# Kernel optimization log

Hardware: AMD Instinct MI355X
Metric: run time of the kernel (lower is better)

The kernel has to match this reference:

```python
import jax, jax.numpy as jnp
import numpy as np

M, N, IN_DIM, NITER = 32, 32, 1024, 100
ALPHA, SIGMA = 0.3, 16.0  # sigma default = max(m, n) / 2
BATCH = 16384


def setup_inputs() -> dict:
    key = jax.random.key(0)
    k1, k2 = jax.random.split(key)
    x = jax.random.normal(k1, (BATCH, IN_DIM), dtype=jnp.float32)
    weights = jax.random.normal(k2, (IN_DIM, M * N), dtype=jnp.float32)
    ii, jj = jnp.meshgrid(jnp.arange(M), jnp.arange(N), indexing='ij')
    locations = jnp.stack([ii.ravel(), jj.ravel()], axis=1).astype(jnp.int32)  # (m*n, 2), row-major like the generator
    return {"x": x, "weights": weights, "locations": locations, "current_iter": 10}


def reference(x, weights, locations, current_iter):
    # x: (B, in_dim); weights: (in_dim, m*n); locations: (m*n, 2)
    B = x.shape[0]
    # Euclidean distances from each sample to each neuron, via ||a-b||^2 expansion
    x2 = jnp.sum(x * x, axis=1, keepdims=True)            # (B, 1)
    w2 = jnp.sum(weights * weights, axis=0)[None, :]      # (1, m*n)
    d2 = jnp.clip(x2 + w2 - 2.0 * (x @ weights), 0.0, None)
    dists = jnp.sqrt(d2)                                  # (B, m*n)
    loss_per = jnp.min(dists, axis=1)                     # (B,)
    bmu_index = jnp.argmin(dists, axis=1)                 # (B,)
    iter_correction = 1.0 - current_iter / NITER
    lr = ALPHA * iter_correction
    sigma = SIGMA * iter_correction
    loc_f = locations.astype(jnp.float32)                 # (m*n, 2)
    bmu_loc = loc_f[bmu_index]                            # (B, 2)
    # squared grid distance of every neuron to each sample's BMU
    dsq = jnp.sum((loc_f[None, :, :] - bmu_loc[:, None, :]) ** 2, axis=2)  # (B, m*n)
    lr_locations = jnp.exp(-dsq / (sigma * sigma)) * lr   # (B, m*n)
    # delta[i,k] = (1/B) * sum_b lr_locations[b,k] * (x[b,i] - weights[i,k])
    # computed without materializing the (B, in_dim, m*n) broadcast tensor
    pos = jnp.einsum('bk,bi->ik', lr_locations, x)        # (in_dim, m*n)
    neg = weights * jnp.sum(lr_locations, axis=0)[None, :]
    delta = (pos - neg) / B
    new_weights = weights + delta
    loss = jnp.sum(loss_per) / B
    return loss, new_weights
```

## Files before the change

### kernel.cpp

```cpp
#include <hip/hip_runtime.h>

typedef unsigned short u16;
typedef short bf16x8 __attribute__((ext_vector_type(8)));
typedef float f32x4 __attribute__((ext_vector_type(4)));

#define BATCH   16384
#define INDIM   1024
#define KNEUR   1024

__device__ __forceinline__ u16 f2bf(float f) {
  union { float f; unsigned u; } v; v.f = f;
  unsigned r = v.u + 0x7FFFu + ((v.u >> 16) & 1u);
  return (u16)(r >> 16);
}
__device__ __forceinline__ float bf2f(u16 h) {
  union { unsigned u; float f; } v; v.u = ((unsigned)h) << 16; return v.f;
}

#define GLDS(gp, lp) __builtin_amdgcn_global_load_lds( \
  (const __attribute__((address_space(1))) void*)(gp), \
  (__attribute__((address_space(3))) void*)(lp), 16, 0, 0)

#define RAWBAR() __builtin_amdgcn_s_barrier()
#define LGKM0() do { asm volatile("s_waitcnt lgkmcnt(0)" ::: "memory"); \
                     __builtin_amdgcn_sched_barrier(0); } while (0)
#define LGKM8() asm volatile("s_waitcnt lgkmcnt(8)" ::: "memory")
#define VMC6() asm volatile("s_waitcnt vmcnt(6)" ::: "memory")
#define VMC0() asm volatile("s_waitcnt vmcnt(0)" ::: "memory")

__global__ __launch_bounds__(256)
void k_prep(const float* __restrict__ x, u16* __restrict__ xb, float* __restrict__ x2,
            const float* __restrict__ w, u16* __restrict__ wt, float* __restrict__ w2,
            const int* __restrict__ loc, const int* __restrict__ itp,
            u16* __restrict__ Tb, float* __restrict__ Tf,
            float* __restrict__ Xf, int* __restrict__ cntcur, float* __restrict__ S) {
  __shared__ float tile[64][65];
  __shared__ float red[4][64];
  int bid = blockIdx.x;
  int t = threadIdx.x;
  if (bid < 4096) {
    int row = bid * 4 + (t >> 6);
    int l = t & 63;
    const float* xr = x + (size_t)row * INDIM;
    u16* xbr = xb + (size_t)row * INDIM;
    float s = 0.f;
    #pragma unroll
    for (int seg = 0; seg < 4; ++seg) {
      float4 v = *(const float4*)(xr + seg * 256 + l * 4);
      ushort4 o; o.x = f2bf(v.x); o.y = f2bf(v.y); o.z = f2bf(v.z); o.w = f2bf(v.w);
      *(ushort4*)(xbr + seg * 256 + l * 4) = o;
      s += v.x * v.x + v.y * v.y + v.z * v.z + v.w * v.w;
    }
    for (int m = 32; m; m >>= 1) s += __shfl_xor(s, m, 64);
    if (l == 0) x2[row] = s;
  } else if (bid < 8192) {
    int id = (bid - 4096) * 256 + t;
    int c = id >> 10, k = id & 1023;
    float corr = 1.f - (float)itp[0] / 100.f;
    float lr = 0.3f * corr;
    float sig = 16.f * corr;
    float inv_s2 = 1.f / (sig * sig);
    int di = loc[2 * c] - loc[2 * k];
    int dj = loc[2 * c + 1] - loc[2 * k + 1];
    float v = lr * __expf(-(float)(di * di + dj * dj) * inv_s2);
    Tf[id] = v;
    Tb[id] = f2bf(v);
    Xf[id] = 0.f;
    if (id < 2304) cntcur[id] = 0;
    if (id < 1024) S[id] = 0.f;
  } else if (bid < 8448) {
    int bb = bid - 8192;
    int bi = bb & 15;
    int bj = bb >> 4;
    int tx = t & 63, ty = t >> 6;
    int i0 = bj * 64, k0 = bi * 64;
    for (int r = ty; r < 64; r += 4)
      tile[r][tx] = w[(size_t)(i0 + r) * KNEUR + k0 + tx];
    __syncthreads();
    for (int r = ty; r < 64; r += 4)
      wt[(size_t)(k0 + r) * INDIM + i0 + tx] = f2bf(tile[tx][r]);
  } else {
    int tx = t & 63, ty = t >> 6;
    int k = (bid - 8448) * 64 + tx;
    float s = 0.f;
    for (int i = ty * 256; i < ty * 256 + 256; ++i) {
      float v = w[(size_t)i * KNEUR + k];
      s += v * v;
    }
    red[ty][tx] = s;
    __syncthreads();
    if (ty == 0) w2[k] = red[0][tx] + red[1][tx] + red[2][tx] + red[3][tx];
  }
}

__global__ __launch_bounds__(512, 2)
void k_gemm1_8p(const u16* __restrict__ A, const u16* __restrict__ Bm,
                const float* __restrict__ x2, const float* __restrict__ w2,
                float* __restrict__ pmin, int* __restrict__ pidx) {
  __shared__ __align__(16) u16 lds[2][2][2][128 * 64];
  __shared__ float s_rv[2][256];
  __shared__ int   s_ri[2][256];

  int bid = blockIdx.x;
  int swz = (bid & 7) * 32 + (bid >> 3);
  int mb = swz >> 2, nb = swz & 3;
  int tid = threadIdx.x;
  int lane = tid & 63;
  int wm = (tid >> 6) >> 1, wn = (tid >> 6) & 1;

  const size_t rowA0 = (size_t)mb * 256;
  const size_t rowB0 = (size_t)nb * 256;

  auto STAGE = [&](int u, int op, int qh) {
    if (u >= 16) return;
    const u16* src = (op == 0) ? (A + (rowA0 + qh * 128) * 1024)
                               : (Bm + (rowB0 + qh * 128) * 1024);
    int k0 = u * 64;
    u16* dst0 = &lds[u & 1][op][qh][0];
    #pragma unroll
    for (int j = 0; j < 2; ++j) {
      int s = j * 512 + tid;
      int r = s >> 3;
      int cs = (s & 7) ^ (r & 7);
      GLDS(src + (size_t)r * 1024 + k0 + cs * 8, dst0 + (size_t)s * 8);
    }
  };
  auto LDA = [&](bf16x8 (&a)[2][2], int db, int qm) {
    #pragma unroll
    for (int mt = 0; mt < 2; ++mt)
      #pragma unroll
      for (int kk = 0; kk < 2; ++kk) {
        int row = wm * 32 + mt * 16 + (lane & 15);
        int ch = (kk * 4 + (lane >> 4)) ^ (row & 7);
        a[mt][kk] = *(const bf16x8*)(&lds[db][0][qm][row * 64 + ch * 8]);
      }
  };
  auto LDB = [&](bf16x8 (&b)[4][2], int db, int qn) {
    #pragma unroll
    for (int nt = 0; nt < 4; ++nt)
      #pragma unroll
      for (int kk = 0; kk < 2; ++kk) {
        int row = wn * 64 + nt * 16 + (lane & 15);
        int ch = (kk * 4 + (lane >> 4)) ^ (row & 7);
        b[nt][kk] = *(const bf16x8*)(&lds[db][1][qn][row * 64 + ch * 8]);
      }
  };

  f32x4 acc[2][2][2][4];
  #pragma unroll
  for (int i = 0; i < 2; ++i)
    #pragma unroll
    for (int j = 0; j < 2; ++j)
      #pragma unroll
      for (int m = 0; m < 2; ++m)
        #pragma unroll
        for (int n = 0; n < 4; ++n) {
          acc[i][j][m][n][0] = 0.f; acc[i][j][m][n][1] = 0.f;
          acc[i][j][m][n][2] = 0.f; acc[i][j][m][n][3] = 0.f;
        }

  bf16x8 a[2][2], b0[4][2], b1[4][2];

  #define PHASE(accq, av, bv) do { \
    __builtin_amdgcn_s_setprio(1); \
    _Pragma("unroll") \
    for (int mt = 0; mt < 2; ++mt) \
      _Pragma("unroll") \
      for (int nt = 0; nt < 4; ++nt) \
        _Pragma("unroll") \
        for (int kk = 0; kk < 2; ++kk) \
          accq[mt][nt] = __builtin_amdgcn_mfma_f32_16x16x32_bf16(av[mt][kk], bv[nt][kk], accq[mt][nt], 0, 0, 0); \
    __builtin_amdgcn_s_setprio(0); \
  } while (0)

  STAGE(0, 0, 0); STAGE(0, 1, 1); STAGE(0, 0, 1); STAGE(0, 1, 0);
  STAGE(1, 0, 0); STAGE(1, 1, 1); STAGE(1, 0, 1);
  VMC6();
  RAWBAR();

  for (int t = 0; t < 16; ++t) {
    int db = t & 1;
    LDA(a, db, 0); LDB(b0, db, 0);
    STAGE(t + 1, 1, 0);
    LGKM8();
    RAWBAR(); LGKM0();
    PHASE(acc[0][0], a, b0);
    RAWBAR();
    LDB(b1, db, 1);
    STAGE(t + 2, 0, 0);
    RAWBAR(); LGKM0();
    PHASE(acc[0][1], a, b1);
    RAWBAR();
    LDA(a, db, 1);
    STAGE(t + 2, 1, 1);
    RAWBAR(); LGKM0();
    PHASE(acc[1][1], a, b1);
    RAWBAR();
    STAGE(t + 2, 0, 1);
    RAWBAR(); LGKM0();
    PHASE(acc[1][0], a, b0);
    if (t < 14) { VMC6(); } else { VMC0(); }
    RAWBAR();
  }

  int g = lane >> 4, li = lane & 15;
  #pragma unroll
  for (int qm = 0; qm < 2; ++qm)
    #pragma unroll
    for (int mt = 0; mt < 2; ++mt)
      #pragma unroll
      for (int rr = 0; rr < 4; ++rr) {
        int lrow = qm * 128 + wm * 32 + mt * 16 + g * 4 + rr;
        float xv = x2[rowA0 + lrow];
        float v = 1e30f; int vi = 0x7fffffff;
        #pragma unroll
        for (int qn = 0; qn < 2; ++qn)
          #pragma unroll
          for (int nt = 0; nt < 4; ++nt) {
            int col = (int)rowB0 + qn * 128 + wn * 64 + nt * 16 + li;
            float d2 = xv + w2[col] - 2.f * acc[qm][qn][mt][nt][rr];
            if (d2 < v) { v = d2; vi = col; }
          }
        #pragma unroll
        for (int m = 1; m < 16; m <<= 1) {
          float ov = __shfl_xor(v, m, 64);
          int oi = __shfl_xor(vi, m, 64);
          if (ov < v || (ov == v && oi < vi)) { v = ov; vi = oi; }
        }
        if (li == 0) { s_rv[wn][lrow] = v; s_ri[wn][lrow] = vi; }
      }
  __syncthreads();
  if (tid < 256) {
    float v0 = s_rv[0][tid], v1 = s_rv[1][tid];
    int i0 = s_ri[0][tid], i1 = s_ri[1][tid];
    float v = v0; int vi = i0;
    if (v1 < v0 || (v1 == v0 && i1 < i0)) { v = v1; vi = i1; }
    size_t brow = rowA0 + tid;
    pmin[brow * 4 + nb] = v;
    pidx[brow * 4 + nb] = vi;
  }
  #undef PHASE
}

__global__ __launch_bounds__(256, 2)
void k_gemm2f(const u16* __restrict__ A, const u16* __restrict__ Bm,
              const float* __restrict__ w, const float* __restrict__ S,
              float* __restrict__ outw) {
  __shared__ __align__(16) u16 ldsA[2][64 * 64];
  __shared__ __align__(16) u16 ldsB[2][64 * 64];

  int bid = blockIdx.x;
  int mb = bid >> 4, nb = bid & 15;
  int tid = threadIdx.x;
  int lane = tid & 63;
  int wid = tid >> 6;
  int wr = wid >> 1, wc = wid & 1;

  const size_t rowA0 = (size_t)mb * 64;
  const size_t rowB0 = (size_t)nb * 64;

  auto STAGE2 = [&](int u, int buf) {
    int k0 = u * 64;
    #pragma unroll
    for (int j = 0; j < 2; ++j) {
      int s = j * 256 + tid;
      int r = s >> 3;
      int cs = (s & 7) ^ (r & 7);
      GLDS(A + (rowA0 + r) * 1024 + k0 + cs * 8, &ldsA[buf][s * 8]);
      GLDS(Bm + (rowB0 + r) * 1024 + k0 + cs * 8, &ldsB[buf][s * 8]);
    }
  };

  f32x4 acc[2][2];
  #pragma unroll
  for (int i = 0; i < 2; ++i)
    #pragma unroll
    for (int j = 0; j < 2; ++j) { acc[i][j][0] = 0.f; acc[i][j][1] = 0.f; acc[i][j][2] = 0.f; acc[i][j][3] = 0.f; }

  STAGE2(0, 0);
  VMC0();
  RAWBAR();

  for (int t = 0; t < 16; ++t) {
    int buf = t & 1;
    if (t < 15) STAGE2(t + 1, buf ^ 1);
    bf16x8 af[2][2], bfr[2][2];
    #pragma unroll
    for (int mt = 0; mt < 2; ++mt)
      #pragma unroll
      for (int kk = 0; kk < 2; ++kk) {
        int row = wr * 32 + mt * 16 + (lane & 15);
        int ch = (kk * 4 + (lane >> 4)) ^ (row & 7);
        af[mt][kk] = *(const bf16x8*)(&ldsA[buf][row * 64 + ch * 8]);
      }
    #pragma unroll
    for (int nt = 0; nt < 2; ++nt)
      #pragma unroll
      for (int kk = 0; kk < 2; ++kk) {
        int row = wc * 32 + nt * 16 + (lane & 15);
        int ch = (kk * 4 + (lane >> 4)) ^ (row & 7);
        bfr[nt][kk] = *(const bf16x8*)(&ldsB[buf][row * 64 + ch * 8]);
      }
    LGKM0();
    __builtin_amdgcn_s_setprio(1);
    #pragma unroll
    for (int mt = 0; mt < 2; ++mt)
      #pragma unroll
      for (int nt = 0; nt < 2; ++nt)
        #pragma unroll
        for (int kk = 0; kk < 2; ++kk)
          acc[mt][nt] = __builtin_amdgcn_mfma_f32_16x16x32_bf16(af[mt][kk], bfr[nt][kk], acc[mt][nt], 0, 0, 0);
    __builtin_amdgcn_s_setprio(0);
    if (t < 15) { VMC0(); RAWBAR(); }
  }

  const float invB = 1.f / (float)BATCH;
  #pragma unroll
  for (int mt = 0; mt < 2; ++mt)
    #pragma unroll
    for (int nt = 0; nt < 2; ++nt)
      #pragma unroll
      for (int r = 0; r < 4; ++r) {
        int i = (int)rowA0 + wr * 32 + mt * 16 + (lane >> 4) * 4 + r;
        int k = (int)rowB0 + wc * 32 + nt * 16 + (lane & 15);
        float wv = w[(size_t)i * KNEUR + k];
        outw[(size_t)i * KNEUR + k] = wv + (acc[mt][nt][r] - wv * S[k]) * invB;
      }
}

__global__ void k_bmu_scan(const float* __restrict__ pmin, const int* __restrict__ pidx,
                           int* __restrict__ bmu, float* __restrict__ lpart,
                           int* __restrict__ cnt, int* __restrict__ ticket,
                           int* __restrict__ cursor, float* __restrict__ cntf,
                           float* __restrict__ out) {
  int t = threadIdx.x;
  int b = blockIdx.x * 256 + t;
  float v = 1e30f; int vi = 0;
  #pragma unroll
  for (int j = 0; j < 4; ++j) {
    float pv = pmin[(size_t)b * 4 + j];
    if (pv < v) { v = pv; vi = pidx[(size_t)b * 4 + j]; }
  }
  bmu[b] = vi;
  atomicAdd(&cnt[vi], 1);
  float d = sqrtf(fmaxf(v, 0.f));
  __shared__ float red[256];
  red[t] = d;
  __syncthreads();
  for (int s = 128; s > 0; s >>= 1) {
    if (t < s) red[t] += red[t + s];
    __syncthreads();
  }
  if (t == 0) lpart[blockIdx.x] = red[0];

  __threadfence();
  __shared__ int is_last;
  if (t == 0) is_last = (atomicAdd(ticket, 1) == 63);
  __syncthreads();
  if (!is_last) return;

  __shared__ int sc[256];
  int4 c4 = *(const int4*)(cnt + 4 * t);
  int tsum = c4.x + c4.y + c4.z + c4.w;
  sc[t] = tsum;
  __syncthreads();
  for (int off = 1; off < 256; off <<= 1) {
    int val = sc[t];
    int add = (t >= off) ? sc[t - off] : 0;
    __syncthreads();
    sc[t] = val + add;
    __syncthreads();
  }
  int excl = sc[t] - tsum;
  cursor[4 * t + 0] = excl;
  cursor[4 * t + 1] = excl + c4.x;
  cursor[4 * t + 2] = excl + c4.x + c4.y;
  cursor[4 * t + 3] = excl + c4.x + c4.y + c4.z;
  cntf[4 * t + 0] = (float)c4.x;
  cntf[4 * t + 1] = (float)c4.y;
  cntf[4 * t + 2] = (float)c4.z;
  cntf[4 * t + 3] = (float)c4.w;
  if (t < 64) {
    float l = lpart[t];
    for (int m = 32; m; m >>= 1) l += __shfl_xor(l, m, 64);
    if (t == 0) out[0] = l * (1.f / (float)BATCH);
  }
}

__global__ void k_place_S(const int* __restrict__ bmu, int* __restrict__ cursor,
                          int* __restrict__ perm,
                          const float* __restrict__ cntf, const float* __restrict__ Tf,
                          float* __restrict__ S) {
  int bid = blockIdx.x;
  int t = threadIdx.x;
  if (bid < 64) {
    int b = bid * 256 + t;
    int c = bmu[b];
    int p = atomicAdd(&cursor[c], 1);
    perm[p] = b;
  } else {
    int chunk = bid - 64;
    int cchunk = chunk >> 2;
    int kb = chunk & 3;
    int k = kb * 256 + t;
    float s = 0.f;
    for (int c = cchunk * 64; c < cchunk * 64 + 64; ++c)
      s += cntf[c] * Tf[(size_t)c * KNEUR + k];
    atomicAdd(&S[k], s);
  }
}

__global__ __launch_bounds__(256)
void k_xsum2(const int* __restrict__ perm, const int* __restrict__ bmu,
             const u16* __restrict__ xb, float* __restrict__ Xf) {
  int t = threadIdx.x;
  int m0 = blockIdx.x * 32;
  int pm[32], cl[32];
  #pragma unroll
  for (int j = 0; j < 32; ++j) pm[j] = perm[m0 + j];
  #pragma unroll
  for (int j = 0; j < 32; ++j) cl[j] = bmu[pm[j]];
  float a0 = 0.f, a1 = 0.f, a2 = 0.f, a3 = 0.f;
  int ccur = cl[0];
  #pragma unroll
  for (int j = 0; j < 32; ++j) {
    if (cl[j] != ccur) {
      float* p = Xf + (size_t)ccur * INDIM + 4 * t;
      atomicAdd(p + 0, a0); atomicAdd(p + 1, a1);
      atomicAdd(p + 2, a2); atomicAdd(p + 3, a3);
      a0 = a1 = a2 = a3 = 0.f;
      ccur = cl[j];
    }
    ushort4 v = *(const ushort4*)(xb + (size_t)pm[j] * INDIM + t * 4);
    a0 += bf2f(v.x); a1 += bf2f(v.y); a2 += bf2f(v.z); a3 += bf2f(v.w);
  }
  float* p = Xf + (size_t)ccur * INDIM + 4 * t;
  atomicAdd(p + 0, a0); atomicAdd(p + 1, a1);
  atomicAdd(p + 2, a2); atomicAdd(p + 3, a3);
}

__global__ void k_trans(const float* __restrict__ Xf, u16* __restrict__ xst) {
  int bid = blockIdx.x;
  int t = threadIdx.x;
  __shared__ float tile[64][65];
  int bc = bid & 15;
  int bi = bid >> 4;
  int tx = t & 63, ty = t >> 6;
  int c0 = bc * 64, i0 = bi * 64;
  for (int r = ty; r < 64; r += 4)
    tile[r][tx] = Xf[(size_t)(c0 + r) * INDIM + i0 + tx];
  __syncthreads();
  for (int r = ty; r < 64; r += 4)
    xst[(size_t)(i0 + r) * KNEUR + c0 + tx] = f2bf(tile[tx][r]);
}

extern "C" void kernel_launch(void* const* d_in, const int* in_sizes, int n_in,
                              void* d_out, int out_size, void* d_ws, size_t ws_size,
                              hipStream_t stream) {
  const float* x = (const float*)d_in[0];
  const float* w = (const float*)d_in[1];
  const int* loc = (const int*)d_in[2];
  const int* it = (const int*)d_in[3];
  float* out = (float*)d_out;

  char* ws = (char*)d_ws;
  size_t off = 0;
  auto alloc = [&](size_t bytes) -> void* {
    void* p = ws + off;
    off += (bytes + 255) & ~(size_t)255;
    return p;
  };
  u16* xb    = (u16*)  alloc((size_t)BATCH * INDIM * 2);
  u16* wt    = (u16*)  alloc((size_t)KNEUR * INDIM * 2);
  u16* Tb    = (u16*)  alloc((size_t)KNEUR * KNEUR * 2);
  float* Tf  = (float*)alloc((size_t)KNEUR * KNEUR * 4);
  u16* xst   = (u16*)  alloc((size_t)INDIM * KNEUR * 2);
  float* x2  = (float*)alloc((size_t)BATCH * 4);
  float* w2  = (float*)alloc((size_t)KNEUR * 4);
  float* pmin= (float*)alloc((size_t)BATCH * 4 * 4);
  int* pidx  = (int*)  alloc((size_t)BATCH * 4 * 4);
  int* bmu   = (int*)  alloc((size_t)BATCH * 4);
  float* cntf= (float*)alloc((size_t)KNEUR * 4);
  float* S   = (float*)alloc((size_t)KNEUR * 4);
  float* lpart=(float*)alloc(64 * 4);
  float* Xf  = (float*)alloc((size_t)KNEUR * INDIM * 4);
  int* cntcur= (int*)  alloc((size_t)2304 * 4);
  int* perm  = (int*)  alloc((size_t)BATCH * 4);
  if (off > ws_size) return;

  int* cnt = cntcur;
  int* cursor = cntcur + KNEUR;
  int* ticket = cntcur + 2 * KNEUR;
  float* outw = out + 1;

  k_prep<<<8464, 256, 0, stream>>>(x, xb, x2, w, wt, w2, loc, it, Tb, Tf, Xf, cntcur, S);
  k_gemm1_8p<<<256, 512, 0, stream>>>(xb, wt, x2, w2, pmin, pidx);
  k_bmu_scan<<<64, 256, 0, stream>>>(pmin, pidx, bmu, lpart, cnt, ticket, cursor, cntf, out);
  k_place_S<<<128, 256, 0, stream>>>(bmu, cursor, perm, cntf, Tf, S);
  k_xsum2<<<BATCH / 32, 256, 0, stream>>>(perm, bmu, xb, Xf);
  k_trans<<<256, 256, 0, stream>>>(Xf, xst);
  k_gemm2f<<<256, 256, 0, stream>>>(xst, Tb, w, S, outw);
}
```

Measured before the change: 135.1 us.

## Quantize x and weights to FP8 e4m3 for the distance GEMM and x sums

The prep kernel now encodes x and the transposed weights as FP8 e4m3 with a software encoder, replacing bf16. The distance GEMM loads 16-byte FP8 chunks into half-size LDS tiles with an adjusted swizzle and uses 16x16x32 fp8 MFMAs. Launch bounds now ask for 4 blocks per CU, and wait counts are retuned for one global-to-LDS load per stage. The x column-sum kernel reads the FP8 copy, so traffic halves and MFMA throughput rises. In exchange, the much coarser precision can flip BMU argmin choices and add error to the weight update.

```diff
diff --git a/kernel.cpp b/kernel.cpp
--- a/kernel.cpp
+++ b/kernel.cpp
@@ -1,6 +1,7 @@
 #include <hip/hip_runtime.h>
 
 typedef unsigned short u16;
+typedef unsigned char u8;
 typedef short bf16x8 __attribute__((ext_vector_type(8)));
 typedef float f32x4 __attribute__((ext_vector_type(4)));
 
@@ -17,6 +18,32 @@
   union { unsigned u; float f; } v; v.u = ((unsigned)h) << 16; return v.f;
 }
 
+__device__ __forceinline__ u8 f2fp8(float f) {
+  float af = fabsf(f);
+  unsigned sign = (__float_as_uint(f) >> 24) & 0x80u;
+  if (af >= 448.f) return (u8)(sign | 0x7E);
+  if (af < 0.015625f) {
+    int q = (int)rintf(af * 512.f);
+    return (u8)(sign | (unsigned)q);
+  }
+  unsigned b = __float_as_uint(af);
+  int e = (int)((b >> 23) & 0xFF) - 127;
+  unsigned m = b & 0x7FFFFFu;
+  unsigned keep = m >> 20;
+  unsigned rest = m & 0xFFFFFu;
+  keep += (rest > 0x80000u) || (rest == 0x80000u && (keep & 1u));
+  unsigned ef = (unsigned)(e + 7);
+  if (keep == 8u) { keep = 0u; ef++; }
+  if (ef >= 16u) return (u8)(sign | 0x7E);
+  return (u8)(sign | (ef << 3) | keep);
+}
+__device__ __forceinline__ float fp8dec(u8 v) {
+  int e = (v >> 3) & 15, m = v & 7;
+  float mag = e ? (float)(8 + m) * __uint_as_float((unsigned)(e + 117) << 23)
+                : (float)m * 0x1p-9f;
+  return (v & 0x80) ? -mag : mag;
+}
+
 #define GLDS(gp, lp) __builtin_amdgcn_global_load_lds( \
   (const __attribute__((address_space(1))) void*)(gp), \
   (__attribute__((address_space(3))) void*)(lp), 16, 0, 0)
@@ -24,13 +51,12 @@
 #define RAWBAR() __builtin_amdgcn_s_barrier()
 #define LGKM0() do { asm volatile("s_waitcnt lgkmcnt(0)" ::: "memory"); \
                      __builtin_amdgcn_sched_barrier(0); } while (0)
-#define LGKM8() asm volatile("s_waitcnt lgkmcnt(8)" ::: "memory")
-#define VMC6() asm volatile("s_waitcnt vmcnt(6)" ::: "memory")
+#define VMC3() asm volatile("s_waitcnt vmcnt(3)" ::: "memory")
 #define VMC0() asm volatile("s_waitcnt vmcnt(0)" ::: "memory")
 
 __global__ __launch_bounds__(256)
-void k_prep(const float* __restrict__ x, u16* __restrict__ xb, float* __restrict__ x2,
-            const float* __restrict__ w, u16* __restrict__ wt, float* __restrict__ w2,
+void k_prep(const float* __restrict__ x, u8* __restrict__ xb, float* __restrict__ x2,
+            const float* __restrict__ w, u8* __restrict__ wt, float* __restrict__ w2,
             const int* __restrict__ loc, const int* __restrict__ itp,
             u16* __restrict__ Tb, float* __restrict__ Tf,
             float* __restrict__ Xf, int* __restrict__ cntcur, float* __restrict__ S) {
@@ -42,13 +68,13 @@
     int row = bid * 4 + (t >> 6);
     int l = t & 63;
     const float* xr = x + (size_t)row * INDIM;
-    u16* xbr = xb + (size_t)row * INDIM;
+    u8* xbr = xb + (size_t)row * INDIM;
     float s = 0.f;
     #pragma unroll
     for (int seg = 0; seg < 4; ++seg) {
       float4 v = *(const float4*)(xr + seg * 256 + l * 4);
-      ushort4 o; o.x = f2bf(v.x); o.y = f2bf(v.y); o.z = f2bf(v.z); o.w = f2bf(v.w);
-      *(ushort4*)(xbr + seg * 256 + l * 4) = o;
+      uchar4 o; o.x = f2fp8(v.x); o.y = f2fp8(v.y); o.z = f2fp8(v.z); o.w = f2fp8(v.w);
+      *(uchar4*)(xbr + seg * 256 + l * 4) = o;
       s += v.x * v.x + v.y * v.y + v.z * v.z + v.w * v.w;
     }
     for (int m = 32; m; m >>= 1) s += __shfl_xor(s, m, 64);
@@ -78,7 +104,7 @@
       tile[r][tx] = w[(size_t)(i0 + r) * KNEUR + k0 + tx];
     __syncthreads();
     for (int r = ty; r < 64; r += 4)
-      wt[(size_t)(k0 + r) * INDIM + i0 + tx] = f2bf(tile[tx][r]);
+      wt[(size_t)(k0 + r) * INDIM + i0 + tx] = f2fp8(tile[tx][r]);
   } else {
     int tx = t & 63, ty = t >> 6;
     int k = (bid - 8448) * 64 + tx;
@@ -93,11 +119,11 @@
   }
 }
 
-__global__ __launch_bounds__(512, 2)
-void k_gemm1_8p(const u16* __restrict__ A, const u16* __restrict__ Bm,
+__global__ __launch_bounds__(512, 4)
+void k_gemm1_8p(const u8* __restrict__ A, const u8* __restrict__ Bm,
                 const float* __restrict__ x2, const float* __restrict__ w2,
                 float* __restrict__ pmin, int* __restrict__ pidx) {
-  __shared__ __align__(16) u16 lds[2][2][2][128 * 64];
+  __shared__ __align__(16) u8 lds[2][2][2][128 * 64];
   __shared__ float s_rv[2][256];
   __shared__ int   s_ri[2][256];
 
@@ -113,37 +139,29 @@
 
   auto STAGE = [&](int u, int op, int qh) {
     if (u >= 16) return;
-    const u16* src = (op == 0) ? (A + (rowA0 + qh * 128) * 1024)
-                               : (Bm + (rowB0 + qh * 128) * 1024);
+    const u8* src = (op == 0) ? (A + (rowA0 + qh * 128) * 1024)
+                              : (Bm + (rowB0 + qh * 128) * 1024);
     int k0 = u * 64;
-    u16* dst0 = &lds[u & 1][op][qh][0];
-    #pragma unroll
-    for (int j = 0; j < 2; ++j) {
-      int s = j * 512 + tid;
-      int r = s >> 3;
-      int cs = (s & 7) ^ (r & 7);
-      GLDS(src + (size_t)r * 1024 + k0 + cs * 8, dst0 + (size_t)s * 8);
+    u8* dst0 = &lds[u & 1][op][qh][0];
+    int r = tid >> 2;
+    int cs = (tid & 3) ^ ((r >> 1) & 3);
+    GLDS(src + (size_t)r * 1024 + k0 + cs * 16, dst0 + (size_t)tid * 16);
+  };
+  auto LDA = [&](long2 (&a)[2], int db, int qm) {
+    #pragma unroll
+    for (int mt = 0; mt < 2; ++mt) {
+      int row = wm * 32 + mt * 16 + (lane & 15);
+      int ch = (lane >> 4) ^ ((row >> 1) & 3);
+      a[mt] = *(const long2*)(&lds[db][0][qm][row * 64 + ch * 16]);
     }
   };
-  auto LDA = [&](bf16x8 (&a)[2][2], int db, int qm) {
-    #pragma unroll
-    for (int mt = 0; mt < 2; ++mt)
-      #pragma unroll
-      for (int kk = 0; kk < 2; ++kk) {
-        int row = wm * 32 + mt * 16 + (lane & 15);
-        int ch = (kk * 4 + (lane >> 4)) ^ (row & 7);
-        a[mt][kk] = *(const bf16x8*)(&lds[db][0][qm][row * 64 + ch * 8]);
-      }
-  };
-  auto LDB = [&](bf16x8 (&b)[4][2], int db, int qn) {
-    #pragma unroll
-    for (int nt = 0; nt < 4; ++nt)
-      #pragma unroll
-      for (int kk = 0; kk < 2; ++kk) {
-        int row = wn * 64 + nt * 16 + (lane & 15);
-        int ch = (kk * 4 + (lane >> 4)) ^ (row & 7);
-        b[nt][kk] = *(const bf16x8*)(&lds[db][1][qn][row * 64 + ch * 8]);
-      }
+  auto LDB = [&](long2 (&b)[4], int db, int qn) {
+    #pragma unroll
+    for (int nt = 0; nt < 4; ++nt) {
+      int row = wn * 64 + nt * 16 + (lane & 15);
+      int ch = (lane >> 4) ^ ((row >> 1) & 3);
+      b[nt] = *(const long2*)(&lds[db][1][qn][row * 64 + ch * 16]);
+    }
   };
 
   f32x4 acc[2][2][2][4];
@@ -159,30 +177,29 @@
           acc[i][j][m][n][2] = 0.f; acc[i][j][m][n][3] = 0.f;
         }
 
-  bf16x8 a[2][2], b0[4][2], b1[4][2];
+  long2 a[2], b0[4], b1[4];
 
   #define PHASE(accq, av, bv) do { \
     __builtin_amdgcn_s_setprio(1); \
     _Pragma("unroll") \
     for (int mt = 0; mt < 2; ++mt) \
       _Pragma("unroll") \
-      for (int nt = 0; nt < 4; ++nt) \
-        _Pragma("unroll") \
-        for (int kk = 0; kk < 2; ++kk) \
-          accq[mt][nt] = __builtin_amdgcn_mfma_f32_16x16x32_bf16(av[mt][kk], bv[nt][kk], accq[mt][nt], 0, 0, 0); \
+      for (int nt = 0; nt < 4; ++nt) { \
+        accq[mt][nt] = __builtin_amdgcn_mfma_f32_16x16x32_fp8_fp8(av[mt].x, bv[nt].x, accq[mt][nt], 0, 0, 0); \
+        accq[mt][nt] = __builtin_amdgcn_mfma_f32_16x16x32_fp8_fp8(av[mt].y, bv[nt].y, accq[mt][nt], 0, 0, 0); \
+      } \
     __builtin_amdgcn_s_setprio(0); \
   } while (0)
 
   STAGE(0, 0, 0); STAGE(0, 1, 1); STAGE(0, 0, 1); STAGE(0, 1, 0);
   STAGE(1, 0, 0); STAGE(1, 1, 1); STAGE(1, 0, 1);
-  VMC6();
+  VMC3();
   RAWBAR();
 
   for (int t = 0; t < 16; ++t) {
     int db = t & 1;
     LDA(a, db, 0); LDB(b0, db, 0);
     STAGE(t + 1, 1, 0);
-    LGKM8();
     RAWBAR(); LGKM0();
     PHASE(acc[0][0], a, b0);
     RAWBAR();
@@ -199,7 +216,7 @@
     STAGE(t + 2, 0, 1);
     RAWBAR(); LGKM0();
     PHASE(acc[1][0], a, b0);
-    if (t < 14) { VMC6(); } else { VMC0(); }
+    if (t < 14) { VMC3(); } else { VMC0(); }
     RAWBAR();
   }
 
@@ -412,7 +429,7 @@
 
 __global__ __launch_bounds__(256)
 void k_xsum2(const int* __restrict__ perm, const int* __restrict__ bmu,
-             const u16* __restrict__ xb, float* __restrict__ Xf) {
+             const u8* __restrict__ xb, float* __restrict__ Xf) {
   int t = threadIdx.x;
   int m0 = blockIdx.x * 32;
   int pm[32], cl[32];
@@ -431,8 +448,8 @@
       a0 = a1 = a2 = a3 = 0.f;
       ccur = cl[j];
     }
-    ushort4 v = *(const ushort4*)(xb + (size_t)pm[j] * INDIM + t * 4);
-    a0 += bf2f(v.x); a1 += bf2f(v.y); a2 += bf2f(v.z); a3 += bf2f(v.w);
+    uchar4 v = *(const uchar4*)(xb + (size_t)pm[j] * INDIM + t * 4);
+    a0 += fp8dec(v.x); a1 += fp8dec(v.y); a2 += fp8dec(v.z); a3 += fp8dec(v.w);
   }
   float* p = Xf + (size_t)ccur * INDIM + 4 * t;
   atomicAdd(p + 0, a0); atomicAdd(p + 1, a1);
@@ -470,8 +487,8 @@
     off += (bytes + 255) & ~(size_t)255;
     return p;
   };
-  u16* xb    = (u16*)  alloc((size_t)BATCH * INDIM * 2);
-  u16* wt    = (u16*)  alloc((size_t)KNEUR * INDIM * 2);
+  u8* xb     = (u8*)   alloc((size_t)BATCH * INDIM);
+  u8* wt     = (u8*)   alloc((size_t)KNEUR * INDIM);
   u16* Tb    = (u16*)  alloc((size_t)KNEUR * KNEUR * 2);
   float* Tf  = (float*)alloc((size_t)KNEUR * KNEUR * 4);
   u16* xst   = (u16*)  alloc((size_t)INDIM * KNEUR * 2);
```

New measurement: 257.0 us. +90.3%, slower.
